# Kernel tuning notes

Measured on AMD Instinct MI355X. Metric: run time of the kernel, lower is better.

The kernel has to match this reference:

```python
import jax, jax.numpy as jnp
import numpy as np

B, S, D, SIZE = 32, 2048, 1024, 1024

def setup_inputs() -> dict:
    key = jax.random.key(0)
    k1, k2, k3, k4, k5 = jax.random.split(key, 5)
    return {
        "inputs": jax.random.normal(k1, (B, S, D), dtype=jnp.float32),
        "g": jax.random.normal(k2, (B, D), dtype=jnp.float32),
        "WO": jax.random.normal(k3, (SIZE, D), dtype=jnp.float32) * 0.05,
        "WG": jax.random.normal(k4, (SIZE, D), dtype=jnp.float32) * 0.05,
        "v": jax.random.normal(k5, (1, SIZE), dtype=jnp.float32) * 0.05,
    }

def reference(inputs, g, WO, WG, v):
    # term1[b,s,k] = WO @ inputs[b,s]; term2[b,k] = WG @ g[b]
    term1 = jnp.einsum('kd,bsd->bsk', WO, inputs)
    term2 = jnp.einsum('kd,bd->bk', WG, g)
    tan_sum = jnp.tanh(term1 + term2[:, None, :])  # [B,S,SIZE]
    # final[b,s] = v @ tan_sum[b,s]  (v is [1,SIZE]); squeeze -> [B,S]
    return jnp.einsum('k,bsk->bs', v[0], tan_sum)
```

## Files before the change

### kernel.cpp

```cpp
#include <hip/hip_runtime.h>
#include <hip/hip_bf16.h>

#define BB   32
#define SS   2048
#define DD   1024
#define SZ   1024
#define MM   (BB*SS)

typedef short bf16x8 __attribute__((ext_vector_type(8)));
typedef float f32x4  __attribute__((ext_vector_type(4)));

__device__ __forceinline__ unsigned short f2bf(float x) {
    unsigned u = __float_as_uint(x);
    u += 0x7fffu + ((u >> 16) & 1u);
    return (unsigned short)(u >> 16);
}
__device__ __forceinline__ unsigned pack2_bf16(float a, float b) {
    return (unsigned)f2bf(a) | ((unsigned)f2bf(b) << 16);
}

__device__ __forceinline__ float ftanh(float x) {
    float e = __expf(2.0f * x);
    return 1.0f - 2.0f / (e + 1.0f);
}

__global__ void prep_kernel(const float* __restrict__ WO,
                            const float* __restrict__ WG,
                            const float* __restrict__ g,
                            unsigned short* __restrict__ WOb,
                            float* __restrict__ term2) {
    __shared__ float gs[DD];
    int bid = blockIdx.x, tid = threadIdx.x;
    if (bid < 1024) {
        int q = bid;
        int d = tid * 4;
        float4 w = *(const float4*)(WO + (size_t)q * DD + d);
        unsigned p0 = pack2_bf16(w.x, w.y), p1 = pack2_bf16(w.z, w.w);
        int dst = ((d >> 5) * 4096 + ((d >> 3) & 3) * 1024 + q) * 8 + (d & 7);
        *(uint2*)&WOb[dst] = make_uint2(p0, p1);
    } else {
        int id = bid - 1024;
        int b  = id >> 2;
        int k  = ((id & 3) << 8) + tid;
        #pragma unroll
        for (int r = 0; r < 4; r++) gs[r * 256 + tid] = g[b * DD + r * 256 + tid];
        __syncthreads();
        const float* wr = WG + (size_t)k * DD;
        float s = 0.f;
        #pragma unroll 4
        for (int d = 0; d < DD; d += 4) {
            float4 wv = *(const float4*)(wr + d);
            s += wv.x * gs[d] + wv.y * gs[d + 1] + wv.z * gs[d + 2] + wv.w * gs[d + 3];
        }
        term2[b * SZ + k] = s;
    }
}

__global__ __launch_bounds__(256, 2) void fused_main(
    const float* __restrict__ Ain,
    const unsigned short* __restrict__ WOb,
    const float* __restrict__ term2,
    const float* __restrict__ v,
    float* __restrict__ out) {
    __shared__ unsigned short Asm[2 * 4096];
    __shared__ unsigned short Bsm[2 * 8192];
    __shared__ float part[2][128];

    const int tid  = threadIdx.x;
    const int wave = tid >> 6;
    const int lane = tid & 63;
    const int wm  = wave & 1, wn = wave >> 1;
    const int l15 = lane & 15;
    const int kgl = lane >> 4;

    const int bid     = blockIdx.x;
    const int logical = (bid & 7) * 256 + (bid >> 3);
    const int ntile = logical & 3;
    const int mtile = logical >> 2;
    const int m0 = mtile * 128;
    const int n0 = ntile * 256;
    const int bidx = m0 >> 11;

    const int rowb = tid >> 3;
    const int sub  = tid & 7;
    const int kgA  = sub >> 1, halfA = sub & 1;

    f32x4 acc[4][8];
    #pragma unroll
    for (int i = 0; i < 4; i++)
        #pragma unroll
        for (int j = 0; j < 8; j++) acc[i][j] = (f32x4){0.f, 0.f, 0.f, 0.f};

    float4 areg[4];

    auto LOAD_A = [&](int k0) {
        #pragma unroll
        for (int r = 0; r < 4; r++) {
            int row = r * 32 + rowb;
            areg[r] = *(const float4*)(Ain + (size_t)(m0 + row) * DD + k0 + sub * 4);
        }
    };
    auto WRITE_A = [&](int buf) {
        #pragma unroll
        for (int r = 0; r < 4; r++) {
            int row = r * 32 + rowb;
            unsigned p0 = pack2_bf16(areg[r].x, areg[r].y);
            unsigned p1 = pack2_bf16(areg[r].z, areg[r].w);
            *(uint2*)&Asm[buf * 4096 + (kgA * 128 + row) * 8 + halfA * 4] =
                make_uint2(p0, p1);
        }
    };
    auto STAGE_B = [&](int buf, int k0) {
        const int dstep = k0 >> 5;
        #pragma unroll
        for (int r = 0; r < 4; r++) {
            const unsigned short* src = WOb + dstep * 32768 + r * 8192 + (n0 + tid) * 8;
            __builtin_amdgcn_global_load_lds(
                (const __attribute__((address_space(1))) void*)src,
                (__attribute__((address_space(3))) void*)(&Bsm[buf * 8192 + (r * 256 + tid) * 8]),
                16, 0, 0);
        }
    };
    auto COMPUTE = [&](int buf) {
        bf16x8 afr[4], bfr[8];
        const int aoff = (kgl * 128 + wm * 64 + l15) * 8;
        const int boff = (kgl * 256 + wn * 128 + l15) * 8;
        #pragma unroll
        for (int mi = 0; mi < 4; mi++)
            afr[mi] = *(const bf16x8*)&Asm[buf * 4096 + aoff + mi * 128];
        #pragma unroll
        for (int ni = 0; ni < 8; ni++)
            bfr[ni] = *(const bf16x8*)&Bsm[buf * 8192 + boff + ni * 128];
        __builtin_amdgcn_s_setprio(1);
        #pragma unroll
        for (int ni = 0; ni < 8; ni++)
            #pragma unroll
            for (int mi = 0; mi < 4; mi++)
                acc[mi][ni] = __builtin_amdgcn_mfma_f32_16x16x32_bf16(
                    afr[mi], bfr[ni], acc[mi][ni], 0, 0, 0);
        __builtin_amdgcn_s_setprio(0);
    };

    LOAD_A(0);
    STAGE_B(0, 0);
    WRITE_A(0);
    __syncthreads();

    for (int t = 0; t < 31; ++t) {
        const int cur = t & 1;
        LOAD_A((t + 1) << 5);
        STAGE_B(cur ^ 1, (t + 1) << 5);
        COMPUTE(cur);
        WRITE_A(cur ^ 1);
        __syncthreads();
    }
    COMPUTE(1);

    float rsum[4][4];
    #pragma unroll
    for (int mi = 0; mi < 4; mi++)
        #pragma unroll
        for (int r = 0; r < 4; r++) rsum[mi][r] = 0.f;

    #pragma unroll
    for (int ni = 0; ni < 8; ni++) {
        int gn = n0 + wn * 128 + ni * 16 + l15;
        float t2 = term2[bidx * SZ + gn];
        float vv = v[gn];
        #pragma unroll
        for (int mi = 0; mi < 4; mi++)
            #pragma unroll
            for (int r = 0; r < 4; r++)
                rsum[mi][r] += ftanh(acc[mi][ni][r] + t2) * vv;
    }
    #pragma unroll
    for (int mi = 0; mi < 4; mi++)
        #pragma unroll
        for (int r = 0; r < 4; r++) {
            float s = rsum[mi][r];
            s += __shfl_xor(s, 1, 16);
            s += __shfl_xor(s, 2, 16);
            s += __shfl_xor(s, 4, 16);
            s += __shfl_xor(s, 8, 16);
            rsum[mi][r] = s;
        }
    float val = 0.f;
    #pragma unroll
    for (int mi = 0; mi < 4; mi++)
        #pragma unroll
        for (int r = 0; r < 4; r++)
            if (l15 == mi * 4 + r) val = rsum[mi][r];
    {
        int mi = l15 >> 2, r = l15 & 3;
        part[wn][wm * 64 + mi * 16 + kgl * 4 + r] = val;
    }
    __syncthreads();
    if (tid < 128) atomicAdd(&out[m0 + tid], part[0][tid] + part[1][tid]);
}

extern "C" void kernel_launch(void* const* d_in, const int* in_sizes, int n_in,
                              void* d_out, int out_size, void* d_ws, size_t ws_size,
                              hipStream_t stream) {
    const float* inputs = (const float*)d_in[0];
    const float* g      = (const float*)d_in[1];
    const float* WO     = (const float*)d_in[2];
    const float* WG     = (const float*)d_in[3];
    const float* v      = (const float*)d_in[4];
    float* out = (float*)d_out;

    unsigned short* WOb = (unsigned short*)d_ws;
    float* term2 = (float*)((char*)d_ws + (size_t)SZ * DD * 2);

    (void)hipMemsetAsync(d_out, 0, sizeof(float) * MM, stream);
    prep_kernel<<<1024 + 128, 256, 0, stream>>>(WO, WG, g, WOb, term2);
    fused_main<<<(MM / 128) * (SZ / 256), 256, 0, stream>>>(inputs, WOb, term2, v, out);
}
```

Before: 575.0 us.

## Deepen A prefetch pipeline with explicit waitcnts and coalesce term2 GEMV

The main GEMM loop is restructured so the A tile is loaded from global memory two steps ahead, kept in registers and written to LDS at the start of the next iteration. Explicit vmcnt/lgkmcnt waits with sched_barriers replace __syncthreads, so the B global_load_lds is waited on while the next A load stays in flight. Separately, the term2 GEMV now uses one wavefront per output row, with coalesced float4 loads and a shuffle reduction, and four times as many blocks. The hand-written waitcnt counts rely on the exact order of outstanding loads, and the last iteration reloads a redundant A tile.

```diff
diff --git a/kernel.cpp b/kernel.cpp
--- a/kernel.cpp
+++ b/kernel.cpp
@@ -29,7 +29,6 @@
                             const float* __restrict__ g,
                             unsigned short* __restrict__ WOb,
                             float* __restrict__ term2) {
-    __shared__ float gs[DD];
     int bid = blockIdx.x, tid = threadIdx.x;
     if (bid < 1024) {
         int q = bid;
@@ -39,20 +38,31 @@
         int dst = ((d >> 5) * 4096 + ((d >> 3) & 3) * 1024 + q) * 8 + (d & 7);
         *(uint2*)&WOb[dst] = make_uint2(p0, p1);
     } else {
-        int id = bid - 1024;
-        int b  = id >> 2;
-        int k  = ((id & 3) << 8) + tid;
-        #pragma unroll
-        for (int r = 0; r < 4; r++) gs[r * 256 + tid] = g[b * DD + r * 256 + tid];
-        __syncthreads();
-        const float* wr = WG + (size_t)k * DD;
-        float s = 0.f;
-        #pragma unroll 4
-        for (int d = 0; d < DD; d += 4) {
-            float4 wv = *(const float4*)(wr + d);
-            s += wv.x * gs[d] + wv.y * gs[d + 1] + wv.z * gs[d + 2] + wv.w * gs[d + 3];
-        }
-        term2[b * SZ + k] = s;
+        int id    = bid - 1024;
+        int b     = id >> 4;
+        int wave  = tid >> 6, lane = tid & 63;
+        int kbase = (id & 15) * 64 + wave * 16;
+        const float* gr = g + (size_t)b * DD + lane * 16;
+        float4 g0 = *(const float4*)(gr + 0);
+        float4 g1 = *(const float4*)(gr + 4);
+        float4 g2 = *(const float4*)(gr + 8);
+        float4 g3 = *(const float4*)(gr + 12);
+        #pragma unroll
+        for (int i = 0; i < 16; i++) {
+            int k = kbase + i;
+            const float* wr = WG + (size_t)k * DD + lane * 16;
+            float4 a0 = *(const float4*)(wr + 0);
+            float4 a1 = *(const float4*)(wr + 4);
+            float4 a2 = *(const float4*)(wr + 8);
+            float4 a3 = *(const float4*)(wr + 12);
+            float s = a0.x*g0.x + a0.y*g0.y + a0.z*g0.z + a0.w*g0.w
+                    + a1.x*g1.x + a1.y*g1.y + a1.z*g1.z + a1.w*g1.w
+                    + a2.x*g2.x + a2.y*g2.y + a2.z*g2.z + a2.w*g2.w
+                    + a3.x*g3.x + a3.y*g3.y + a3.z*g3.z + a3.w*g3.w;
+            #pragma unroll
+            for (int m = 1; m < 64; m <<= 1) s += __shfl_xor(s, m);
+            if (lane == 0) term2[b * SZ + k] = s;
+        }
     }
 }
 
@@ -62,8 +72,8 @@
     const float* __restrict__ term2,
     const float* __restrict__ v,
     float* __restrict__ out) {
-    __shared__ unsigned short Asm[2 * 4096];
-    __shared__ unsigned short Bsm[2 * 8192];
+    __shared__ unsigned short Abuf[2][4096];
+    __shared__ unsigned short Bbuf[2][8192];
     __shared__ float part[2][128];
 
     const int tid  = threadIdx.x;
@@ -71,7 +81,7 @@
     const int lane = tid & 63;
     const int wm  = wave & 1, wn = wave >> 1;
     const int l15 = lane & 15;
-    const int kgl = lane >> 4;
+    const int k8  = lane >> 4;
 
     const int bid     = blockIdx.x;
     const int logical = (bid & 7) * 256 + (bid >> 3);
@@ -81,10 +91,6 @@
     const int n0 = ntile * 256;
     const int bidx = m0 >> 11;
 
-    const int rowb = tid >> 3;
-    const int sub  = tid & 7;
-    const int kgA  = sub >> 1, halfA = sub & 1;
-
     f32x4 acc[4][8];
     #pragma unroll
     for (int i = 0; i < 4; i++)
@@ -96,41 +102,40 @@
     auto LOAD_A = [&](int k0) {
         #pragma unroll
         for (int r = 0; r < 4; r++) {
-            int row = r * 32 + rowb;
-            areg[r] = *(const float4*)(Ain + (size_t)(m0 + row) * DD + k0 + sub * 4);
+            int row = r * 32 + (tid >> 3);
+            areg[r] = *(const float4*)(Ain + (size_t)(m0 + row) * DD + k0 + (tid & 7) * 4);
         }
     };
     auto WRITE_A = [&](int buf) {
-        #pragma unroll
-        for (int r = 0; r < 4; r++) {
-            int row = r * 32 + rowb;
+        const int q = tid & 7, kg = q >> 1, half = q & 1;
+        #pragma unroll
+        for (int r = 0; r < 4; r++) {
+            int row = r * 32 + (tid >> 3);
             unsigned p0 = pack2_bf16(areg[r].x, areg[r].y);
             unsigned p1 = pack2_bf16(areg[r].z, areg[r].w);
-            *(uint2*)&Asm[buf * 4096 + (kgA * 128 + row) * 8 + halfA * 4] =
-                make_uint2(p0, p1);
-        }
-    };
-    auto STAGE_B = [&](int buf, int k0) {
-        const int dstep = k0 >> 5;
-        #pragma unroll
-        for (int r = 0; r < 4; r++) {
-            const unsigned short* src = WOb + dstep * 32768 + r * 8192 + (n0 + tid) * 8;
+            *(uint2*)&Abuf[buf][(kg * 128 + row) * 8 + half * 4] = make_uint2(p0, p1);
+        }
+    };
+    auto STAGE_B = [&](int buf, int kt) {
+        #pragma unroll
+        for (int r = 0; r < 4; r++) {
+            const unsigned short* src = WOb + ((size_t)(kt * 4 + r) * 1024 + n0 + tid) * 8;
             __builtin_amdgcn_global_load_lds(
                 (const __attribute__((address_space(1))) void*)src,
-                (__attribute__((address_space(3))) void*)(&Bsm[buf * 8192 + (r * 256 + tid) * 8]),
+                (__attribute__((address_space(3))) void*)(&Bbuf[buf][(r * 256 + tid) * 8]),
                 16, 0, 0);
         }
     };
     auto COMPUTE = [&](int buf) {
         bf16x8 afr[4], bfr[8];
-        const int aoff = (kgl * 128 + wm * 64 + l15) * 8;
-        const int boff = (kgl * 256 + wn * 128 + l15) * 8;
+        const int aoff = (k8 * 128 + wm * 64 + l15) * 8;
+        const int boff = (k8 * 256 + wn * 128 + l15) * 8;
         #pragma unroll
         for (int mi = 0; mi < 4; mi++)
-            afr[mi] = *(const bf16x8*)&Asm[buf * 4096 + aoff + mi * 128];
+            afr[mi] = *(const bf16x8*)&Abuf[buf][aoff + mi * 128];
         #pragma unroll
         for (int ni = 0; ni < 8; ni++)
-            bfr[ni] = *(const bf16x8*)&Bsm[buf * 8192 + boff + ni * 128];
+            bfr[ni] = *(const bf16x8*)&Bbuf[buf][boff + ni * 128];
         __builtin_amdgcn_s_setprio(1);
         #pragma unroll
         for (int ni = 0; ni < 8; ni++)
@@ -142,17 +147,31 @@
     };
 
     LOAD_A(0);
+    WRITE_A(0);
+    __builtin_amdgcn_sched_barrier(0);
     STAGE_B(0, 0);
-    WRITE_A(0);
-    __syncthreads();
+    __builtin_amdgcn_sched_barrier(0);
+    LOAD_A(32);
+    __builtin_amdgcn_sched_barrier(0);
+    asm volatile("s_waitcnt vmcnt(4)" ::: "memory");
+    asm volatile("s_waitcnt lgkmcnt(0)" ::: "memory");
+    __builtin_amdgcn_sched_barrier(0);
+    __builtin_amdgcn_s_barrier();
 
     for (int t = 0; t < 31; ++t) {
-        const int cur = t & 1;
-        LOAD_A((t + 1) << 5);
-        STAGE_B(cur ^ 1, (t + 1) << 5);
-        COMPUTE(cur);
-        WRITE_A(cur ^ 1);
-        __syncthreads();
+        const int buf = t & 1;
+        WRITE_A(buf ^ 1);
+        __builtin_amdgcn_sched_barrier(0);
+        STAGE_B(buf ^ 1, t + 1);
+        __builtin_amdgcn_sched_barrier(0);
+        LOAD_A(((t + 2 <= 31) ? t + 2 : 31) << 5);
+        __builtin_amdgcn_sched_barrier(0);
+        COMPUTE(buf);
+        __builtin_amdgcn_sched_barrier(0);
+        asm volatile("s_waitcnt vmcnt(4)" ::: "memory");
+        asm volatile("s_waitcnt lgkmcnt(0)" ::: "memory");
+        __builtin_amdgcn_sched_barrier(0);
+        __builtin_amdgcn_s_barrier();
     }
     COMPUTE(1);
 
@@ -192,7 +211,7 @@
             if (l15 == mi * 4 + r) val = rsum[mi][r];
     {
         int mi = l15 >> 2, r = l15 & 3;
-        part[wn][wm * 64 + mi * 16 + kgl * 4 + r] = val;
+        part[wn][wm * 64 + mi * 16 + k8 * 4 + r] = val;
     }
     __syncthreads();
     if (tid < 128) atomicAdd(&out[m0 + tid], part[0][tid] + part[1][tid]);
@@ -212,6 +231,6 @@
     float* term2 = (float*)((char*)d_ws + (size_t)SZ * DD * 2);
 
     (void)hipMemsetAsync(d_out, 0, sizeof(float) * MM, stream);
-    prep_kernel<<<1024 + 128, 256, 0, stream>>>(WO, WG, g, WOb, term2);
+    prep_kernel<<<1024 + 512, 256, 0, stream>>>(WO, WG, g, WOb, term2);
     fused_main<<<(MM / 128) * (SZ / 256), 256, 0, stream>>>(inputs, WOb, term2, v, out);
 }
```

Measured after the change: 534.1 us. 1.08x faster.
